# Performance work log

Hardware: AMD Instinct MI355X
Metric: run time of the kernel (lower is better)

The kernel has to match this reference:

```python
import jax, jax.numpy as jnp
import numpy as np


def setup_inputs() -> dict:
    key = jax.random.key(0)
    k1, k2, k3 = jax.random.split(key, 3)
    B, V, J = 32, 100000, 52
    vertices = jax.random.normal(k1, (1, V, 3), dtype=jnp.float32)
    lbs_weights = jax.random.uniform(k2, (1, V, J), dtype=jnp.float32)
    skinning_transforms = jax.random.normal(k3, (B, J, 4, 4), dtype=jnp.float32)
    return {
        "vertices": vertices,
        "lbs_weights": lbs_weights,
        "skinning_transforms": skinning_transforms,
    }


def reference(vertices, lbs_weights, skinning_transforms):
    # 3D-vertices branch of Skinning.forward
    B = skinning_transforms.shape[0]
    J = skinning_transforms.shape[1]
    V = vertices.shape[1]
    # W: [B,V,J] (broadcast of [1,V,J]); T_flat: [B,V,16] -> T: [B,V,4,4]
    T = jnp.einsum(
        "bvj,bjx->bvx",
        jnp.broadcast_to(lbs_weights, (B, V, J)),
        skinning_transforms.reshape(B, J, 16),
    ).reshape(B, V, 4, 4)
    # homogeneous vertex coords [B,V,4]
    v_posed_homo = jnp.concatenate(
        [
            jnp.broadcast_to(vertices, (B, V, 3)),
            jnp.ones((B, V, 1), dtype=vertices.dtype),
        ],
        axis=2,
    )
    # per-vertex 4x4 @ 4 transform, keep xyz
    v_homo = jnp.einsum("bvij,bvj->bvi", T, v_posed_homo)
    return v_homo[:, :, :3]
```

## Files before the change

### kernel.cpp

```cpp
#include <hip/hip_runtime.h>
#include <hip/hip_bf16.h>


typedef __attribute__((ext_vector_type(8))) short bf16x8;
typedef __attribute__((ext_vector_type(4))) float f32x4;

constexpr int J      = 52;
constexpr int NT     = 6;
constexpr int WAVES  = 4;
constexpr int MT     = 2;
constexpr int VPW    = MT * 16;
constexpr int VPB    = WAVES * VPW;
constexpr int KSTEPS = 7;
constexpr int GMAX   = 512;

constexpr int BP_B   = KSTEPS * NT * 64 * 16;
constexpr int SPAD   = 100;
constexpr int SL_B   = 16 * SPAD * 4;
constexpr int NF4    = 32 * J * 4;

__device__ __forceinline__ unsigned pk2(float a, float b) {
    __hip_bfloat162 h = __float22bfloat162_rn(make_float2(a, b));
    return *reinterpret_cast<unsigned*>(&h);
}

__global__ __launch_bounds__(256, 2) void skin_persist(
    const float* __restrict__ verts,
    const float* __restrict__ weights,
    const float* __restrict__ xf,
    float* __restrict__ out,
    int V, int ntiles, int gsize)
{
    __shared__ __align__(16) char sBp[BP_B];
    __shared__ __align__(16) char sSl[WAVES][SL_B];

    const int tid  = threadIdx.x;
    const int lane = tid & 63;
    const int wid  = tid >> 6;
    const int lgrp = lane >> 4;
    const int lrow = lane & 15;

    int tv = blockIdx.x;

    float hx[MT], hy[MT], hz[MT];
    float2 wv[MT][KSTEPS];
#pragma unroll
    for (int mt = 0; mt < MT; ++mt) {
        const int v   = tv * VPB + wid * VPW + mt * 16 + lrow;
        const int vcl = (v < V) ? v : (V - 1);
        hx[mt] = verts[3 * (size_t)vcl + 0];
        hy[mt] = verts[3 * (size_t)vcl + 1];
        hz[mt] = verts[3 * (size_t)vcl + 2];
        const float* wr = weights + (size_t)vcl * J;
#pragma unroll
        for (int s = 0; s < KSTEPS; ++s) {
            const int j0 = s * 8 + lgrp * 2;
            wv[mt][s] = (j0 < J) ? *(const float2*)(wr + j0) : float2{0.f, 0.f};
        }
    }

    {
        const float4* __restrict__ xf4 = reinterpret_cast<const float4*>(xf);
        for (int it = 0; it < NF4 / 256; ++it) {
            const int g = it * 256 + tid;
            const float4 m = xf4[g];
            const int b   = g / 208;
            const int rem = g - b * 208;
            const int j = rem >> 2;
            const int i = rem & 3;
            if (i < 3) {
                const int n    = 3 * b + i;
                const int slot = ((j >> 3) * NT + (n >> 4)) * 64
                               + ((j >> 1) & 3) * 16 + (n & 15);
                uint2 d;
                d.x = pk2(m.x, m.y);
                d.y = pk2(m.z, m.w);
                *(uint2*)(sBp + slot * 16 + (j & 1) * 8) = d;
            }
        }
        for (int z = tid; z < NT * 32; z += 256) {
            const int t = z >> 5, l = z & 31;
            const int slot = (6 * NT + t) * 64 + 32 + l;
            *(f32x4*)(sBp + slot * 16) = f32x4{0.f, 0.f, 0.f, 0.f};
        }
    }
    __syncthreads();

    for (;;) {
        f32x4 acc[MT][NT];
#pragma unroll
        for (int mt = 0; mt < MT; ++mt)
#pragma unroll
            for (int t = 0; t < NT; ++t)
                acc[mt][t] = f32x4{0.f, 0.f, 0.f, 0.f};

#pragma unroll
        for (int s = 0; s < KSTEPS; ++s) {
            bf16x8 frag[NT];
#pragma unroll
            for (int t = 0; t < NT; ++t)
                frag[t] = *(const bf16x8*)(sBp + ((s * NT + t) * 64 + lane) * 16);
#pragma unroll
            for (int mt = 0; mt < MT; ++mt) {
                const float w0 = wv[mt][s].x, w1 = wv[mt][s].y;
                union { bf16x8 v; unsigned w[4]; } xf8;
                xf8.w[0] = pk2(w0 * hx[mt], w0 * hy[mt]);
                xf8.w[1] = pk2(w0 * hz[mt], w0);
                xf8.w[2] = pk2(w1 * hx[mt], w1 * hy[mt]);
                xf8.w[3] = pk2(w1 * hz[mt], w1);
#pragma unroll
                for (int t = 0; t < NT; ++t)
                    acc[mt][t] = __builtin_amdgcn_mfma_f32_16x16x32_bf16(
                        frag[t], xf8.v, acc[mt][t], 0, 0, 0);
            }
        }

        const int v0w = tv * VPB + wid * VPW;
        const long long validf = ((long long)V - v0w) * 3;
        const int tvn = tv + gsize;

        if (tvn < ntiles) {
#pragma unroll
            for (int mt = 0; mt < MT; ++mt) {
                const int v   = tvn * VPB + wid * VPW + mt * 16 + lrow;
                const int vcl = (v < V) ? v : (V - 1);
                hx[mt] = verts[3 * (size_t)vcl + 0];
                hy[mt] = verts[3 * (size_t)vcl + 1];
                hz[mt] = verts[3 * (size_t)vcl + 2];
                const float* wr = weights + (size_t)vcl * J;
#pragma unroll
                for (int s = 0; s < KSTEPS; ++s) {
                    const int j0 = s * 8 + lgrp * 2;
                    wv[mt][s] = (j0 < J) ? *(const float2*)(wr + j0)
                                         : float2{0.f, 0.f};
                }
            }
        }

        char* const sl = sSl[wid];
#pragma unroll
        for (int h = 0; h < 2; ++h) {
#pragma unroll
            for (int mt = 0; mt < MT; ++mt) {
                const int vloc = mt * 16 + lrow;
#pragma unroll
                for (int tt = 0; tt < 3; ++tt) {
                    const int t = 3 * h + tt;
#pragma unroll
                    for (int r = 0; r < 4; ++r) {
                        const int n  = 16 * t + lgrp * 4 + r;
                        const int b  = n / 3;
                        const int i  = n - 3 * b;
                        const int fl = (b - 16 * h) * SPAD + vloc * 3 + i;
                        *(float*)(sl + fl * 4) = acc[mt][t][r];
                    }
                }
            }
            asm volatile("s_waitcnt lgkmcnt(0)" ::: "memory");
            __builtin_amdgcn_sched_barrier(0);

            f32x4 vals[6];
#pragma unroll
            for (int q = 0; q < 6; ++q) {
                const int f  = q * 64 + lane;
                const int bl = f / 24;
                const int rr = f - bl * 24;
                vals[q] = *(const f32x4*)(sl + bl * (SPAD * 4) + rr * 16);
            }
            asm volatile("s_waitcnt lgkmcnt(0)" ::: "memory");
            __builtin_amdgcn_sched_barrier(0);

#pragma unroll
            for (int q = 0; q < 6; ++q) {
                const int f  = q * 64 + lane;
                const int bl = f / 24;
                const int rr = f - bl * 24;
                float* dst = out + (size_t)(16 * h + bl) * (size_t)V * 3
                                 + (size_t)v0w * 3 + rr * 4;
                if ((long long)(rr + 1) * 4 <= validf) {
                    *(float4*)dst = *(const float4*)&vals[q];
                } else if ((long long)rr * 4 < validf) {
#pragma unroll
                    for (int e = 0; e < 4; ++e)
                        if ((long long)(rr * 4 + e) < validf) dst[e] = vals[q][e];
                }
            }
        }

        if (tvn >= ntiles) break;
        tv = tvn;
    }
}

extern "C" void kernel_launch(void* const* d_in, const int* in_sizes, int n_in,
                              void* d_out, int out_size, void* d_ws, size_t ws_size,
                              hipStream_t stream)
{
    const float* verts   = (const float*)d_in[0];
    const float* weights = (const float*)d_in[1];
    const float* xf      = (const float*)d_in[2];
    float* out = (float*)d_out;

    const int V = in_sizes[0] / 3;
    const int ntiles = (V + VPB - 1) / VPB;
    const int G = ntiles < GMAX ? ntiles : GMAX;

    skin_persist<<<G, 256, 0, stream>>>(verts, weights, xf, out, V, ntiles, G);
}
```

Baseline: 24.24 us.

## Stage weights via coalesced float4 loads into per-wave LDS and prefetch next tile

Weight rows are now loaded as contiguous float4 chunks covering each wave's 32 vertices, staged into a per-wave LDS buffer, and the next tile's chunk is prefetched into registers at the start of each iteration. This replaces the earlier strided float2 per-lane global loads with fully coalesced accesses and hides latency behind the MFMA loop. The per-wave LDS region is shared with the output transpose scratch, and the LDS footprint grows (32*52*4 bytes per wave versus 16*100*4 bytes), which may affect occupancy. The design also adds register pressure from the 7 prefetched float4 values.

New measurement: 31.96 us. 31.8% more time.

```diff
diff --git a/kernel.cpp b/kernel.cpp
--- a/kernel.cpp
+++ b/kernel.cpp
@@ -17,6 +17,8 @@
 constexpr int BP_B   = KSTEPS * NT * 64 * 16;
 constexpr int SPAD   = 100;
 constexpr int SL_B   = 16 * SPAD * 4;
+constexpr int WS_B   = VPW * J * 4;
+constexpr int WCH    = VPW * J / 4;
 constexpr int NF4    = 32 * J * 4;
 
 __device__ __forceinline__ unsigned pk2(float a, float b) {
@@ -32,18 +34,30 @@
     int V, int ntiles, int gsize)
 {
     __shared__ __align__(16) char sBp[BP_B];
-    __shared__ __align__(16) char sSl[WAVES][SL_B];
+    __shared__ __align__(16) char sWS[WAVES][WS_B];
 
     const int tid  = threadIdx.x;
     const int lane = tid & 63;
     const int wid  = tid >> 6;
     const int lgrp = lane >> 4;
     const int lrow = lane & 15;
+    char* const sW = sWS[wid];
 
     int tv = blockIdx.x;
 
+    f32x4 wreg[7];
+    {
+        const size_t base = (size_t)(tv * VPB + wid * VPW) * 13;
+        const size_t lim  = (size_t)V * 13 - 1;
+#pragma unroll
+        for (int it = 0; it < 7; ++it) {
+            const int c = it * 64 + lane;
+            size_t fidx = base + (c < WCH ? c : WCH - 1);
+            if (fidx > lim) fidx = lim;
+            wreg[it] = *(const f32x4*)(weights + fidx * 4);
+        }
+    }
     float hx[MT], hy[MT], hz[MT];
-    float2 wv[MT][KSTEPS];
 #pragma unroll
     for (int mt = 0; mt < MT; ++mt) {
         const int v   = tv * VPB + wid * VPW + mt * 16 + lrow;
@@ -51,12 +65,6 @@
         hx[mt] = verts[3 * (size_t)vcl + 0];
         hy[mt] = verts[3 * (size_t)vcl + 1];
         hz[mt] = verts[3 * (size_t)vcl + 2];
-        const float* wr = weights + (size_t)vcl * J;
-#pragma unroll
-        for (int s = 0; s < KSTEPS; ++s) {
-            const int j0 = s * 8 + lgrp * 2;
-            wv[mt][s] = (j0 < J) ? *(const float2*)(wr + j0) : float2{0.f, 0.f};
-        }
     }
 
     {
@@ -84,9 +92,43 @@
             *(f32x4*)(sBp + slot * 16) = f32x4{0.f, 0.f, 0.f, 0.f};
         }
     }
+#pragma unroll
+    for (int it = 0; it < 7; ++it) {
+        const int c = it * 64 + lane;
+        if (c < WCH) *(f32x4*)(sW + c * 16) = wreg[it];
+    }
     __syncthreads();
 
     for (;;) {
+        const int tvn = tv + gsize;
+
+        if (tvn < ntiles) {
+            const size_t base = (size_t)(tvn * VPB + wid * VPW) * 13;
+            const size_t lim  = (size_t)V * 13 - 1;
+#pragma unroll
+            for (int it = 0; it < 7; ++it) {
+                const int c = it * 64 + lane;
+                size_t fidx = base + (c < WCH ? c : WCH - 1);
+                if (fidx > lim) fidx = lim;
+                wreg[it] = *(const f32x4*)(weights + fidx * 4);
+            }
+        }
+
+        asm volatile("s_waitcnt lgkmcnt(0)" ::: "memory");
+        __builtin_amdgcn_sched_barrier(0);
+
+        float2 wv[MT][KSTEPS];
+#pragma unroll
+        for (int mt = 0; mt < MT; ++mt) {
+            const char* rb = sW + ((mt * 16 + lrow) * J) * 4;
+#pragma unroll
+            for (int s = 0; s < KSTEPS; ++s) {
+                const int j0 = s * 8 + lgrp * 2;
+                wv[mt][s] = (j0 < J) ? *(const float2*)(rb + j0 * 4)
+                                     : float2{0.f, 0.f};
+            }
+        }
+
         f32x4 acc[MT][NT];
 #pragma unroll
         for (int mt = 0; mt < MT; ++mt)
@@ -117,8 +159,6 @@
 
         const int v0w = tv * VPB + wid * VPW;
         const long long validf = ((long long)V - v0w) * 3;
-        const int tvn = tv + gsize;
-
         if (tvn < ntiles) {
 #pragma unroll
             for (int mt = 0; mt < MT; ++mt) {
@@ -127,17 +167,10 @@
                 hx[mt] = verts[3 * (size_t)vcl + 0];
                 hy[mt] = verts[3 * (size_t)vcl + 1];
                 hz[mt] = verts[3 * (size_t)vcl + 2];
-                const float* wr = weights + (size_t)vcl * J;
-#pragma unroll
-                for (int s = 0; s < KSTEPS; ++s) {
-                    const int j0 = s * 8 + lgrp * 2;
-                    wv[mt][s] = (j0 < J) ? *(const float2*)(wr + j0)
-                                         : float2{0.f, 0.f};
-                }
-            }
-        }
-
-        char* const sl = sSl[wid];
+            }
+        }
+
+        char* const sl = sW;
 #pragma unroll
         for (int h = 0; h < 2; ++h) {
 #pragma unroll
@@ -188,6 +221,12 @@
         }
 
         if (tvn >= ntiles) break;
+
+#pragma unroll
+        for (int it = 0; it < 7; ++it) {
+            const int c = it * 64 + lane;
+            if (c < WCH) *(f32x4*)(sW + c * 16) = wreg[it];
+        }
         tv = tvn;
     }
 }
```
